# Optimization experiments

Hardware: AMD Instinct MI355X
Metric: run time of the kernel (lower is better)

Reference implementation:

```python
import jax, jax.numpy as jnp
import numpy as np

B, M, IN, H = 4096, 16, 512, 512


def _linear_params(key, out_dim, in_dim):
    kw, kb = jax.random.split(key)
    s = 1.0 / np.sqrt(in_dim)
    W = jax.random.uniform(kw, (out_dim, in_dim), jnp.float32, -s, s)
    b = jax.random.uniform(kb, (out_dim,), jnp.float32, -s, s)
    return W, b


def setup_inputs() -> dict:
    key = jax.random.key(0)
    ks = jax.random.split(key, 15)
    inp = {
        "input": jax.random.normal(ks[0], (B, IN), jnp.float32),
        "h0": jax.random.normal(ks[1], (B, H), jnp.float32),
        "c0": jax.random.normal(ks[2], (B, H), jnp.float32),
        "all_c_b_e_w": jax.random.normal(ks[3], (B, M, H), jnp.float32),
        "all_num_word": jax.random.randint(ks[4], (B,), 0, M + 1, jnp.int32),
    }
    names = ["ii", "hi", "if_", "hf", "ig", "hg", "io", "ho", "lx", "lc"]
    in_dims = [IN, H, IN, H, IN, H, IN, H, IN, H]
    for n, d, k in zip(names, in_dims, ks[5:15]):
        W, b = _linear_params(k, H, d)
        inp["W_" + n] = W
        inp["b_" + n] = b
    return inp


def _lin(x, W, b):
    return x @ W.T + b


def reference(input, h0, c0, all_c_b_e_w, all_num_word,
              W_ii, b_ii, W_hi, b_hi, W_if_, b_if_, W_hf, b_hf,
              W_ig, b_ig, W_hg, b_hg, W_io, b_io, W_ho, b_ho,
              W_lx, b_lx, W_lc, b_lc):
    i = jax.nn.sigmoid(_lin(input, W_ii, b_ii) + _lin(h0, W_hi, b_hi))   # [B,H]
    f = jax.nn.sigmoid(_lin(input, W_if_, b_if_) + _lin(h0, W_hf, b_hf))  # computed but unused, as in original
    g = jnp.tanh(_lin(input, W_ig, b_ig) + _lin(h0, W_hg, b_hg))         # [B,H]
    o = jax.nn.sigmoid(_lin(input, W_io, b_io) + _lin(h0, W_ho, b_ho))   # [B,H]

    # lattice word-cell gates, vectorized over the ragged word dim with a mask
    lx = _lin(input, W_lx, b_lx)                 # [B,H]
    lc = _lin(all_c_b_e_w, W_lc, b_lc)           # [B,M,H]
    i_b = jax.nn.sigmoid(lx[:, None, :] + lc)    # [B,M,H]
    mask = (jnp.arange(M)[None, :] < all_num_word[:, None])  # [B,M]
    exp_b = jnp.exp(i_b) * mask[:, :, None].astype(i_b.dtype)  # [B,M,H]
    exp_i = jnp.exp(i)                                         # [B,H]
    denom = exp_i + jnp.sum(exp_b, axis=1)                     # [B,H]
    c_words = jnp.sum((exp_b / denom[:, None, :]) * all_c_b_e_w, axis=1)
    c_lat = c_words + (exp_i / denom) * g
    c = jnp.where((all_num_word > 0)[:, None], c_lat, g)       # num_word==0 -> c=g
    h1 = o * jnp.tanh(c)
    return (h1, c)
```

## Files before the change

kernel.cpp:

```cpp
#include <hip/hip_runtime.h>
#include <hip/hip_bf16.h>
#include <stdint.h>


typedef __attribute__((ext_vector_type(8))) short short8;
typedef __attribute__((ext_vector_type(4))) float f32x4;
typedef __attribute__((ext_vector_type(4))) unsigned short us4;

__device__ __forceinline__ unsigned short f2bf(float f) {
  union { float f; unsigned u; } v; v.f = f;
  return (unsigned short)((v.u + 0x7fffu + ((v.u >> 16) & 1u)) >> 16);
}
__device__ __forceinline__ unsigned short f2bf_h(float f) {
  __hip_bfloat16 h = __float2bfloat16(f);
  return *reinterpret_cast<unsigned short*>(&h);
}
__device__ __forceinline__ float bf2f(unsigned short u) {
  return __uint_as_float((unsigned)u << 16);
}
__device__ __forceinline__ float sigmoidf_(float x) {
  return 1.f / (1.f + __expf(-x));
}
__device__ __forceinline__ float fast_tanh(float x) {
  float e = __expf(-2.f * fmaxf(x, -30.f));
  return (1.f - e) / (1.f + e);
}

__global__ void k_cvt_xh(const float* __restrict__ x, const float* __restrict__ h,
                         unsigned short* __restrict__ out) {
  int t = blockIdx.x * blockDim.x + threadIdx.x;
  int b = t >> 8;
  int col = (t & 255) * 4;
  const float* src = (col < 512) ? (x + (size_t)b * 512 + col)
                                 : (h + (size_t)b * 512 + (col - 512));
  f32x4 v = *(const f32x4*)src;
  us4 o;
  o[0] = f2bf(v[0]); o[1] = f2bf(v[1]); o[2] = f2bf(v[2]); o[3] = f2bf(v[3]);
  *(us4*)(out + (size_t)t * 4) = o;
}

__global__ void k_cvt_w(const float* __restrict__ Wii, const float* __restrict__ Wig,
                        const float* __restrict__ Wio, const float* __restrict__ Wlx,
                        const float* __restrict__ Whi, const float* __restrict__ Whg,
                        const float* __restrict__ Who, unsigned short* __restrict__ out) {
  int t = blockIdx.x * blockDim.x + threadIdx.x;
  int row = t >> 8;
  int col = (t & 255) * 4;
  int sec = row >> 9, r = row & 511;
  us4 o;
  if (col < 512) {
    const float* W = sec == 0 ? Wii : sec == 1 ? Wig : sec == 2 ? Wio : Wlx;
    f32x4 v = *(const f32x4*)(W + (size_t)r * 512 + col);
    o[0] = f2bf(v[0]); o[1] = f2bf(v[1]); o[2] = f2bf(v[2]); o[3] = f2bf(v[3]);
  } else if (sec < 3) {
    const float* W = sec == 0 ? Whi : sec == 1 ? Whg : Who;
    f32x4 v = *(const f32x4*)(W + (size_t)r * 512 + (col - 512));
    o[0] = f2bf(v[0]); o[1] = f2bf(v[1]); o[2] = f2bf(v[2]); o[3] = f2bf(v[3]);
  } else {
    o[0] = 0; o[1] = 0; o[2] = 0; o[3] = 0;
  }
  *(us4*)(out + (size_t)t * 4) = o;
}

__global__ void k_cvt_wlc(const float* __restrict__ src, unsigned short* __restrict__ out) {
  int t = blockIdx.x * blockDim.x + threadIdx.x;
  f32x4 v = *(const f32x4*)(src + (size_t)t * 4);
  us4 o;
  o[0] = f2bf(v[0]); o[1] = f2bf(v[1]); o[2] = f2bf(v[2]); o[3] = f2bf(v[3]);
  *(us4*)(out + (size_t)t * 4) = o;
}

__global__ __launch_bounds__(256) void k_gemm0(
    const unsigned short* __restrict__ A, const unsigned short* __restrict__ Bm,
    unsigned short* __restrict__ C, int Ndim, int Kdim, int nbx) {
  __shared__ unsigned short As[2][128 * 64];
  __shared__ unsigned short Bs[2][128 * 64];
  const int tid = threadIdx.x;
  const int lane = tid & 63, wid = tid >> 6;
  const int wr = wid >> 1, wc = wid & 1;
  const int l15 = lane & 15, lhi = lane >> 4;

  const int chunk = gridDim.x >> 3;
  const int bid = (blockIdx.x & 7) * chunk + (blockIdx.x >> 3);
  const int brow = bid / nbx, bcol = bid % nbx;
  const int m0 = brow * 128, n0 = bcol * 128;

  f32x4 acc[4][4];
#pragma unroll
  for (int i = 0; i < 4; ++i)
#pragma unroll
    for (int j = 0; j < 4; ++j) acc[i][j] = (f32x4){0.f, 0.f, 0.f, 0.f};

  const int cb0 = wid * 64;
  auto stage = [&](int buf, int k0) {
#pragma unroll
    for (int q = 0; q < 4; ++q) {
      const int cb = q * 256 + cb0;
      const int chunkid = cb + lane;
      const int row = chunkid >> 3, slot = chunkid & 7;
      const int kk = k0 + ((slot ^ (row & 7)) << 3);
      __builtin_amdgcn_global_load_lds(
          (const __attribute__((address_space(1))) unsigned int*)(A + (size_t)(m0 + row) * Kdim + kk),
          (__attribute__((address_space(3))) unsigned int*)(As[buf] + cb * 8), 16, 0, 0);
      __builtin_amdgcn_global_load_lds(
          (const __attribute__((address_space(1))) unsigned int*)(Bm + (size_t)(n0 + row) * Kdim + kk),
          (__attribute__((address_space(3))) unsigned int*)(Bs[buf] + cb * 8), 16, 0, 0);
    }
  };

  const int nt = Kdim >> 6;
  stage(0, 0);
  __syncthreads();

  const int swz = (lane & 7) << 4;
  for (int t = 0; t < nt; ++t) {
    const int cur = t & 1;
    if (t + 1 < nt) stage(cur ^ 1, (t + 1) << 6);
    const char* Ab = (const char*)As[cur];
    const char* Bb = (const char*)Bs[cur];
#pragma unroll
    for (int s = 0; s < 2; ++s) {
      short8 av[4], bv[4];
#pragma unroll
      for (int mi = 0; mi < 4; ++mi) {
        const int row = wr * 64 + mi * 16 + l15;
        av[mi] = *(const short8*)(Ab + row * 128 + ((s * 64 + lhi * 16) ^ swz));
      }
#pragma unroll
      for (int ni = 0; ni < 4; ++ni) {
        const int row = wc * 64 + ni * 16 + l15;
        bv[ni] = *(const short8*)(Bb + row * 128 + ((s * 64 + lhi * 16) ^ swz));
      }
#pragma unroll
      for (int mi = 0; mi < 4; ++mi)
#pragma unroll
        for (int ni = 0; ni < 4; ++ni)
          acc[mi][ni] = __builtin_amdgcn_mfma_f32_16x16x32_bf16(av[mi], bv[ni], acc[mi][ni], 0, 0, 0);
    }
    __syncthreads();
  }

#pragma unroll
  for (int mi = 0; mi < 4; ++mi) {
    const int gr = m0 + wr * 64 + mi * 16 + lhi * 4;
#pragma unroll
    for (int ni = 0; ni < 4; ++ni) {
      const int gc = n0 + wc * 64 + ni * 16 + l15;
#pragma unroll
      for (int j = 0; j < 4; ++j)
        C[(size_t)(gr + j) * Ndim + gc] = f2bf(acc[mi][ni][j]);
    }
  }
}

__global__ __launch_bounds__(512) void k_latg(
    const float* __restrict__ Af,
    const unsigned short* __restrict__ Bm,
    unsigned short* __restrict__ lcb) {
  __shared__ unsigned short As[2][256 * 32];
  __shared__ unsigned short Bs[2][256 * 32];
  const int tid = threadIdx.x;
  const int lane = tid & 63, wid = tid >> 6;
  const int wrow = wid >> 2, wcol = wid & 3;
  const int l15 = lane & 15, lhi = lane >> 4;

  const int chunk = gridDim.x >> 3;
  const int bid = (blockIdx.x & 7) * chunk + (blockIdx.x >> 3);
  const int brow = bid >> 1, bcol = bid & 1;
  const int m0 = brow * 256, n0 = bcol * 256;

  f32x4 acc[8][4];
#pragma unroll
  for (int i = 0; i < 8; ++i)
#pragma unroll
    for (int j = 0; j < 4; ++j) acc[i][j] = (f32x4){0.f, 0.f, 0.f, 0.f};

  f32x4 SA[2][2], SB[2][2];

  auto loadA = [&](f32x4 (&dst)[2][2], int k0) {
#pragma unroll
    for (int q = 0; q < 2; ++q) {
      const int c = q * 512 + tid;
      const int row = c >> 2, s = c & 3;
      const float* p = Af + (size_t)(m0 + row) * 512 + k0 + s * 8;
      dst[q][0] = *(const f32x4*)p;
      dst[q][1] = *(const f32x4*)(p + 4);
    }
  };
  auto writeA = [&](int buf, f32x4 (&src)[2][2]) {
#pragma unroll
    for (int q = 0; q < 2; ++q) {
      const int c = q * 512 + tid;
      const int row = c >> 2, s = c & 3;
      const int pr = row >> 1;
      const int phys = (s + ((row & 1) << 2)) ^ (pr & 7);
      short8 v;
      v[0] = (short)f2bf_h(src[q][0][0]); v[1] = (short)f2bf_h(src[q][0][1]);
      v[2] = (short)f2bf_h(src[q][0][2]); v[3] = (short)f2bf_h(src[q][0][3]);
      v[4] = (short)f2bf_h(src[q][1][0]); v[5] = (short)f2bf_h(src[q][1][1]);
      v[6] = (short)f2bf_h(src[q][1][2]); v[7] = (short)f2bf_h(src[q][1][3]);
      *(short8*)((char*)As[buf] + pr * 128 + phys * 16) = v;
    }
  };
  auto stageB = [&](int buf, int k0) {
#pragma unroll
    for (int q = 0; q < 2; ++q) {
      const int cb = q * 512 + wid * 64;
      const int c = cb + lane;
      const int pr = c >> 3, phys = c & 7;
      const int gi = phys ^ (pr & 7);
      const int row = pr * 2 + (gi >> 2);
      const int kk = k0 + ((gi & 3) << 3);
      __builtin_amdgcn_global_load_lds(
          (const __attribute__((address_space(1))) unsigned int*)(Bm + (size_t)(n0 + row) * 512 + kk),
          (__attribute__((address_space(3))) unsigned int*)(Bs[buf] + cb * 8), 16, 0, 0);
    }
  };

  auto compute = [&](int buf) {
    const char* Ab = (const char*)As[buf];
    const char* Bb = (const char*)Bs[buf];
    short8 av[8], bv[4];
#pragma unroll
    for (int mi = 0; mi < 8; ++mi) {
      const int row = wrow * 128 + mi * 16 + l15;
      const int pr = row >> 1;
      av[mi] = *(const short8*)(Ab + pr * 128 +
                (((lhi + ((row & 1) << 2)) ^ (pr & 7)) << 4));
    }
#pragma unroll
    for (int ni = 0; ni < 4; ++ni) {
      const int row = wcol * 64 + ni * 16 + l15;
      const int pr = row >> 1;
      bv[ni] = *(const short8*)(Bb + pr * 128 +
                (((lhi + ((row & 1) << 2)) ^ (pr & 7)) << 4));
    }
#pragma unroll
    for (int mi = 0; mi < 8; ++mi)
#pragma unroll
      for (int ni = 0; ni < 4; ++ni)
        acc[mi][ni] = __builtin_amdgcn_mfma_f32_16x16x32_bf16(av[mi], bv[ni], acc[mi][ni], 0, 0, 0);
  };

  loadA(SA, 0);
  loadA(SB, 32);
  stageB(0, 0);
  writeA(0, SA);
  __syncthreads();

#pragma unroll 1
  for (int t = 0; t < 16; t += 2) {
    if (t + 2 < 16) loadA(SA, (t + 2) << 5);
    if (t + 1 < 16) stageB(1, (t + 1) << 5);
    compute(0);
    if (t + 1 < 16) writeA(1, SB);
    __syncthreads();
    if (t + 3 < 16) loadA(SB, (t + 3) << 5);
    if (t + 2 < 16) stageB(0, (t + 2) << 5);
    compute(1);
    if (t + 2 < 16) writeA(0, SA);
    __syncthreads();
  }

#pragma unroll
  for (int mi = 0; mi < 8; ++mi) {
    const int gr = m0 + wrow * 128 + mi * 16 + lhi * 4;
#pragma unroll
    for (int ni = 0; ni < 4; ++ni) {
      const int gc = n0 + wcol * 64 + ni * 16 + l15;
#pragma unroll
      for (int j = 0; j < 4; ++j)
        lcb[(size_t)(gr + j) * 512 + gc] = f2bf(acc[mi][ni][j]);
    }
  }
}

__global__ __launch_bounds__(512) void k_epi(
    const unsigned short* __restrict__ lc,
    const float* __restrict__ all_c,
    const unsigned short* __restrict__ C1u,
    const int* __restrict__ num_word,
    const float* __restrict__ b_ii, const float* __restrict__ b_hi,
    const float* __restrict__ b_ig, const float* __restrict__ b_hg,
    const float* __restrict__ b_io, const float* __restrict__ b_ho,
    const float* __restrict__ b_lx, const float* __restrict__ b_lc,
    float* __restrict__ outH, float* __restrict__ outC) {
  const int b = blockIdx.x;
  const int hc = threadIdx.x;
  const int nw = num_word[b];
  const size_t base = (size_t)b * 2048;

  const float pre = bf2f(C1u[base + 1536 + hc]) + b_lx[hc] + b_lc[hc];
  const unsigned short* lcp = lc + ((size_t)b * 16) * 512 + hc;
  const float* wp = all_c + ((size_t)b * 16) * 512 + hc;

  float se = 0.f, sew = 0.f;
#pragma unroll 4
  for (int m = 0; m < nw; ++m) {
    const float ib = sigmoidf_(pre + bf2f(lcp[(size_t)m * 512]));
    const float e = __expf(ib);
    se += e;
    sew += e * wp[(size_t)m * 512];
  }

  const float ig = sigmoidf_(bf2f(C1u[base + hc]) + b_ii[hc] + b_hi[hc]);
  const float g  = fast_tanh(bf2f(C1u[base + 512 + hc]) + b_ig[hc] + b_hg[hc]);
  const float og = sigmoidf_(bf2f(C1u[base + 1024 + hc]) + b_io[hc] + b_ho[hc]);
  const float ei = __expf(ig);
  const float denom = ei + se;
  const float cc = (sew + ei * g) / denom;
  outH[(size_t)b * 512 + hc] = og * fast_tanh(cc);
  outC[(size_t)b * 512 + hc] = cc;
}

extern "C" void kernel_launch(void* const* d_in, const int* in_sizes, int n_in,
                              void* d_out, int out_size, void* d_ws, size_t ws_size,
                              hipStream_t stream) {
  const float* input    = (const float*)d_in[0];
  const float* h0       = (const float*)d_in[1];
  const float* all_c    = (const float*)d_in[3];
  const int*   num_word = (const int*)d_in[4];
  const float* W_ii = (const float*)d_in[5];  const float* b_ii = (const float*)d_in[6];
  const float* W_hi = (const float*)d_in[7];  const float* b_hi = (const float*)d_in[8];
  const float* W_ig = (const float*)d_in[13]; const float* b_ig = (const float*)d_in[14];
  const float* W_hg = (const float*)d_in[15]; const float* b_hg = (const float*)d_in[16];
  const float* W_io = (const float*)d_in[17]; const float* b_io = (const float*)d_in[18];
  const float* W_ho = (const float*)d_in[19]; const float* b_ho = (const float*)d_in[20];
  const float* W_lx = (const float*)d_in[21]; const float* b_lx = (const float*)d_in[22];
  const float* W_lc = (const float*)d_in[23]; const float* b_lc = (const float*)d_in[24];

  char* ws = (char*)d_ws;
  unsigned short* XH   = (unsigned short*)(ws);
  unsigned short* Wcat = (unsigned short*)(ws + 8388608);
  unsigned short* Wlc  = (unsigned short*)(ws + 12582912);
  unsigned short* C1u  = (unsigned short*)(ws + 13107200);
  unsigned short* lc   = (unsigned short*)(ws + 29884416);

  float* outH = (float*)d_out;
  float* outC = outH + (size_t)4096 * 512;

  k_cvt_xh<<<4096, 256, 0, stream>>>(input, h0, XH);
  k_cvt_w<<<2048, 256, 0, stream>>>(W_ii, W_ig, W_io, W_lx, W_hi, W_hg, W_ho, Wcat);
  k_cvt_wlc<<<256, 256, 0, stream>>>(W_lc, Wlc);

  k_gemm0<<<512, 256, 0, stream>>>(XH, Wcat, C1u, 2048, 1024, 16);

  k_latg<<<512, 512, 0, stream>>>(all_c, Wlc, lc);

  k_epi<<<4096, 512, 0, stream>>>(lc, all_c, C1u, num_word,
      b_ii, b_hi, b_ig, b_hg, b_io, b_ho, b_lx, b_lc, outH, outC);
}
```

Measured before the change: 116.0 us.

## Fuse lattice epilogue into lc GEMM and merge conversion kernels

The lattice-cell epilogue (sigmoid, exp, masked softmax-like reduction over words, gate math) now runs directly on the k_latg accumulator registers, reducing across the 16 word rows with cross-lane shuffles. This removes the bf16 lc intermediate (a 64MB-scale write and reread) and the separate k_epi launch. The three fp32-to-bf16 conversion kernels are merged into one launch. In exchange, the GEMM epilogue does more work and register pressure rises. The accumulator is also used at full precision instead of rounded to bf16.

New measurement: 138.8 us. +19.7%, slower.

```diff
diff --git a/kernel.cpp b/kernel.cpp
--- a/kernel.cpp
+++ b/kernel.cpp
@@ -26,48 +26,48 @@
   return (1.f - e) / (1.f + e);
 }
 
-__global__ void k_cvt_xh(const float* __restrict__ x, const float* __restrict__ h,
-                         unsigned short* __restrict__ out) {
-  int t = blockIdx.x * blockDim.x + threadIdx.x;
-  int b = t >> 8;
-  int col = (t & 255) * 4;
-  const float* src = (col < 512) ? (x + (size_t)b * 512 + col)
-                                 : (h + (size_t)b * 512 + (col - 512));
-  f32x4 v = *(const f32x4*)src;
+__global__ void k_cvt_all(const float* __restrict__ x, const float* __restrict__ h,
+                          const float* __restrict__ Wii, const float* __restrict__ Wig,
+                          const float* __restrict__ Wio, const float* __restrict__ Wlx,
+                          const float* __restrict__ Whi, const float* __restrict__ Whg,
+                          const float* __restrict__ Who, const float* __restrict__ Wlcf,
+                          unsigned short* __restrict__ XH, unsigned short* __restrict__ Wcat,
+                          unsigned short* __restrict__ Wlc) {
+  const int bb = blockIdx.x;
+  const int tid = threadIdx.x;
   us4 o;
-  o[0] = f2bf(v[0]); o[1] = f2bf(v[1]); o[2] = f2bf(v[2]); o[3] = f2bf(v[3]);
-  *(us4*)(out + (size_t)t * 4) = o;
-}
-
-__global__ void k_cvt_w(const float* __restrict__ Wii, const float* __restrict__ Wig,
-                        const float* __restrict__ Wio, const float* __restrict__ Wlx,
-                        const float* __restrict__ Whi, const float* __restrict__ Whg,
-                        const float* __restrict__ Who, unsigned short* __restrict__ out) {
-  int t = blockIdx.x * blockDim.x + threadIdx.x;
-  int row = t >> 8;
-  int col = (t & 255) * 4;
-  int sec = row >> 9, r = row & 511;
-  us4 o;
-  if (col < 512) {
-    const float* W = sec == 0 ? Wii : sec == 1 ? Wig : sec == 2 ? Wio : Wlx;
-    f32x4 v = *(const f32x4*)(W + (size_t)r * 512 + col);
+  if (bb < 4096) {
+    const int t = bb * 256 + tid;
+    const int b = t >> 8;
+    const int col = (t & 255) * 4;
+    const float* src = (col < 512) ? (x + (size_t)b * 512 + col)
+                                   : (h + (size_t)b * 512 + (col - 512));
+    f32x4 v = *(const f32x4*)src;
     o[0] = f2bf(v[0]); o[1] = f2bf(v[1]); o[2] = f2bf(v[2]); o[3] = f2bf(v[3]);
-  } else if (sec < 3) {
-    const float* W = sec == 0 ? Whi : sec == 1 ? Whg : Who;
-    f32x4 v = *(const f32x4*)(W + (size_t)r * 512 + (col - 512));
+    *(us4*)(XH + (size_t)t * 4) = o;
+  } else if (bb < 6144) {
+    const int t = (bb - 4096) * 256 + tid;
+    const int row = t >> 8;
+    const int col = (t & 255) * 4;
+    const int sec = row >> 9, r = row & 511;
+    if (col < 512) {
+      const float* W = sec == 0 ? Wii : sec == 1 ? Wig : sec == 2 ? Wio : Wlx;
+      f32x4 v = *(const f32x4*)(W + (size_t)r * 512 + col);
+      o[0] = f2bf(v[0]); o[1] = f2bf(v[1]); o[2] = f2bf(v[2]); o[3] = f2bf(v[3]);
+    } else if (sec < 3) {
+      const float* W = sec == 0 ? Whi : sec == 1 ? Whg : Who;
+      f32x4 v = *(const f32x4*)(W + (size_t)r * 512 + (col - 512));
+      o[0] = f2bf(v[0]); o[1] = f2bf(v[1]); o[2] = f2bf(v[2]); o[3] = f2bf(v[3]);
+    } else {
+      o[0] = 0; o[1] = 0; o[2] = 0; o[3] = 0;
+    }
+    *(us4*)(Wcat + (size_t)t * 4) = o;
+  } else {
+    const int t = (bb - 6144) * 256 + tid;
+    f32x4 v = *(const f32x4*)(Wlcf + (size_t)t * 4);
     o[0] = f2bf(v[0]); o[1] = f2bf(v[1]); o[2] = f2bf(v[2]); o[3] = f2bf(v[3]);
-  } else {
-    o[0] = 0; o[1] = 0; o[2] = 0; o[3] = 0;
-  }
-  *(us4*)(out + (size_t)t * 4) = o;
-}
-
-__global__ void k_cvt_wlc(const float* __restrict__ src, unsigned short* __restrict__ out) {
-  int t = blockIdx.x * blockDim.x + threadIdx.x;
-  f32x4 v = *(const f32x4*)(src + (size_t)t * 4);
-  us4 o;
-  o[0] = f2bf(v[0]); o[1] = f2bf(v[1]); o[2] = f2bf(v[2]); o[3] = f2bf(v[3]);
-  *(us4*)(out + (size_t)t * 4) = o;
+    *(us4*)(Wlc + (size_t)t * 4) = o;
+  }
 }
 
 __global__ __launch_bounds__(256) void k_gemm0(
@@ -156,7 +156,13 @@
 __global__ __launch_bounds__(512) void k_latg(
     const float* __restrict__ Af,
     const unsigned short* __restrict__ Bm,
-    unsigned short* __restrict__ lcb) {
+    const unsigned short* __restrict__ C1u,
+    const int* __restrict__ num_word,
+    const float* __restrict__ b_ii, const float* __restrict__ b_hi,
+    const float* __restrict__ b_ig, const float* __restrict__ b_hg,
+    const float* __restrict__ b_io, const float* __restrict__ b_ho,
+    const float* __restrict__ b_lx, const float* __restrict__ b_lc,
+    float* __restrict__ outH, float* __restrict__ outC) {
   __shared__ unsigned short As[2][256 * 32];
   __shared__ unsigned short Bs[2][256 * 32];
   const int tid = threadIdx.x;
@@ -262,55 +268,46 @@
     __syncthreads();
   }
 
-#pragma unroll
-  for (int mi = 0; mi < 8; ++mi) {
-    const int gr = m0 + wrow * 128 + mi * 16 + lhi * 4;
-#pragma unroll
-    for (int ni = 0; ni < 4; ++ni) {
-      const int gc = n0 + wcol * 64 + ni * 16 + l15;
-#pragma unroll
-      for (int j = 0; j < 4; ++j)
-        lcb[(size_t)(gr + j) * 512 + gc] = f2bf(acc[mi][ni][j]);
-    }
-  }
-}
-
-__global__ __launch_bounds__(512) void k_epi(
-    const unsigned short* __restrict__ lc,
-    const float* __restrict__ all_c,
-    const unsigned short* __restrict__ C1u,
-    const int* __restrict__ num_word,
-    const float* __restrict__ b_ii, const float* __restrict__ b_hi,
-    const float* __restrict__ b_ig, const float* __restrict__ b_hg,
-    const float* __restrict__ b_io, const float* __restrict__ b_ho,
-    const float* __restrict__ b_lx, const float* __restrict__ b_lc,
-    float* __restrict__ outH, float* __restrict__ outC) {
-  const int b = blockIdx.x;
-  const int hc = threadIdx.x;
-  const int nw = num_word[b];
-  const size_t base = (size_t)b * 2048;
-
-  const float pre = bf2f(C1u[base + 1536 + hc]) + b_lx[hc] + b_lc[hc];
-  const unsigned short* lcp = lc + ((size_t)b * 16) * 512 + hc;
-  const float* wp = all_c + ((size_t)b * 16) * 512 + hc;
-
-  float se = 0.f, sew = 0.f;
-#pragma unroll 4
-  for (int m = 0; m < nw; ++m) {
-    const float ib = sigmoidf_(pre + bf2f(lcp[(size_t)m * 512]));
-    const float e = __expf(ib);
-    se += e;
-    sew += e * wp[(size_t)m * 512];
-  }
-
-  const float ig = sigmoidf_(bf2f(C1u[base + hc]) + b_ii[hc] + b_hi[hc]);
-  const float g  = fast_tanh(bf2f(C1u[base + 512 + hc]) + b_ig[hc] + b_hg[hc]);
-  const float og = sigmoidf_(bf2f(C1u[base + 1024 + hc]) + b_io[hc] + b_ho[hc]);
-  const float ei = __expf(ig);
-  const float denom = ei + se;
-  const float cc = (sew + ei * g) / denom;
-  outH[(size_t)b * 512 + hc] = og * fast_tanh(cc);
-  outC[(size_t)b * 512 + hc] = cc;
+  const int b0 = m0 >> 4;
+#pragma unroll
+  for (int ni = 0; ni < 4; ++ni) {
+    const int hc = n0 + wcol * 64 + ni * 16 + l15;
+    const float pre0 = b_lx[hc] + b_lc[hc];
+    const float bI = b_ii[hc] + b_hi[hc];
+    const float bG = b_ig[hc] + b_hg[hc];
+    const float bO = b_io[hc] + b_ho[hc];
+#pragma unroll
+    for (int mi = 0; mi < 8; ++mi) {
+      const int b = b0 + wrow * 8 + mi;
+      const int nw = num_word[b];
+      const size_t base = (size_t)b * 2048;
+      const float pre = bf2f(C1u[base + 1536 + hc]) + pre0;
+      float se = 0.f, sew = 0.f;
+#pragma unroll
+      for (int j = 0; j < 4; ++j) {
+        const int m = lhi * 4 + j;
+        const float ib = sigmoidf_(pre + acc[mi][ni][j]);
+        const float e = (m < nw) ? __expf(ib) : 0.f;
+        const float w = Af[((size_t)b * 16 + m) * 512 + hc];
+        se += e;
+        sew += e * w;
+      }
+      se += __shfl_xor(se, 16, 64);
+      sew += __shfl_xor(sew, 16, 64);
+      se += __shfl_xor(se, 32, 64);
+      sew += __shfl_xor(sew, 32, 64);
+      if (lhi == 0) {
+        const float ig = sigmoidf_(bf2f(C1u[base + hc]) + bI);
+        const float g  = fast_tanh(bf2f(C1u[base + 512 + hc]) + bG);
+        const float og = sigmoidf_(bf2f(C1u[base + 1024 + hc]) + bO);
+        const float ei = __expf(ig);
+        const float denom = ei + se;
+        const float cc = (sew + ei * g) / denom;
+        outH[(size_t)b * 512 + hc] = og * fast_tanh(cc);
+        outC[(size_t)b * 512 + hc] = cc;
+      }
+    }
+  }
 }
 
 extern "C" void kernel_launch(void* const* d_in, const int* in_sizes, int n_in,
@@ -334,19 +331,15 @@
   unsigned short* Wcat = (unsigned short*)(ws + 8388608);
   unsigned short* Wlc  = (unsigned short*)(ws + 12582912);
   unsigned short* C1u  = (unsigned short*)(ws + 13107200);
-  unsigned short* lc   = (unsigned short*)(ws + 29884416);
 
   float* outH = (float*)d_out;
   float* outC = outH + (size_t)4096 * 512;
 
-  k_cvt_xh<<<4096, 256, 0, stream>>>(input, h0, XH);
-  k_cvt_w<<<2048, 256, 0, stream>>>(W_ii, W_ig, W_io, W_lx, W_hi, W_hg, W_ho, Wcat);
-  k_cvt_wlc<<<256, 256, 0, stream>>>(W_lc, Wlc);
+  k_cvt_all<<<6400, 256, 0, stream>>>(input, h0, W_ii, W_ig, W_io, W_lx,
+                                      W_hi, W_hg, W_ho, W_lc, XH, Wcat, Wlc);
 
   k_gemm0<<<512, 256, 0, stream>>>(XH, Wcat, C1u, 2048, 1024, 16);
 
-  k_latg<<<512, 512, 0, stream>>>(all_c, Wlc, lc);
-
-  k_epi<<<4096, 512, 0, stream>>>(lc, all_c, C1u, num_word,
+  k_latg<<<512, 512, 0, stream>>>(all_c, Wlc, C1u, num_word,
       b_ii, b_hi, b_ig, b_hg, b_io, b_ho, b_lx, b_lc, outH, outC);
 }
```
